# Optimization experiments

Measured on AMD Instinct MI355X. Metric: run time of the kernel, lower is better.

The kernel has to match this reference:

```python
import jax, jax.numpy as jnp
import numpy as np

B, T, D_IN, D_H, D_OUT = 32, 2048, 1024, 1024, 1024

def setup_inputs() -> dict:
    key = jax.random.key(0)
    k1, k2, k3, k4, k5 = jax.random.split(key, 5)
    s = jax.random.normal(k1, (B, D_IN), dtype=jnp.float32)
    h = jax.random.normal(k2, (B, T, D_H), dtype=jnp.float32)
    # params (original uses np.random.random, i.e. uniform [0,1); scale kept modest)
    W_a = jax.random.uniform(k3, (D_IN, D_OUT), dtype=jnp.float32)
    U_a = jax.random.uniform(k4, (D_H, D_OUT), dtype=jnp.float32)
    v_a = jax.random.uniform(k5, (D_OUT,), dtype=jnp.float32)
    return {"s": s, "h": h, "W_a": W_a, "U_a": U_a, "v_a": v_a}

def reference(s, h, W_a, U_a, v_a):
    # Bahdanau additive attention:
    # e_bt = v_a . tanh(s W_a + h_t U_a);  a = softmax_t(e);  c_b = sum_t a_bt h_bt
    u_a_h = jnp.einsum('bth,ho->bto', h, U_a)            # [B,T,O]
    w_a_s = jnp.einsum('bi,io->bo', s, W_a)[:, None, :]  # [B,1,O]
    e = jnp.einsum('bto,o->bt', jnp.tanh(w_a_s + u_a_h), v_a)  # [B,T]
    a = jax.nn.softmax(e, axis=-1)                       # [B,T]
    c = jnp.einsum('bt,bth->bh', a, h)                   # [B,H]
    return c
```

## Files before the change

### kernel.cpp

```cpp
#include <hip/hip_runtime.h>
#include <hip/hip_bf16.h>
#include <stdint.h>

#define Bb 32
#define Tt 2048
#define Dd 1024

typedef float    f32x4 __attribute__((ext_vector_type(4)));
typedef _Float16 f16x8 __attribute__((ext_vector_type(8)));
typedef uint32_t u32;

#define WS_A     131072
#define WS_EP    393216
#define WS_UT    4587520

__device__ __forceinline__ void gll16(const void* g, const void* lds) {
  __builtin_amdgcn_global_load_lds(
      (const __attribute__((address_space(1))) u32*)(uintptr_t)g,
      (__attribute__((address_space(3))) u32*)(uint32_t)(uintptr_t)lds,
      16, 0, 0);
}

__global__ __launch_bounds__(256) void k_ws(const float* __restrict__ s,
                                            const float* __restrict__ W,
                                            float* __restrict__ w2_ws) {
  const int b = blockIdx.x >> 2;
  const int o = (blockIdx.x & 3) * 256 + threadIdx.x;
  __shared__ float s_sh[Dd];
#pragma unroll
  for (int j = 0; j < 4; ++j)
    s_sh[threadIdx.x + 256 * j] = s[b * Dd + threadIdx.x + 256 * j];
  __syncthreads();
  float acc = 0.f;
#pragma unroll 8
  for (int i = 0; i < Dd; ++i) acc += s_sh[i] * W[(size_t)i * Dd + o];
  w2_ws[b * Dd + o] = 2.f * acc;
}

__global__ __launch_bounds__(256) void k_ut(const float* __restrict__ U,
                                            uint8_t* __restrict__ U_ts) {
  const int i0 = (blockIdx.x >> 4) * 64;
  const int o0 = (blockIdx.x & 15) * 64;
  __shared__ float tile[64][65];
  const int tx = threadIdx.x & 63;
  const int ty = threadIdx.x >> 6;
#pragma unroll
  for (int jj = 0; jj < 16; ++jj)
    tile[tx][ty + 4 * jj] = U[(size_t)(i0 + ty + 4 * jj) * Dd + o0 + tx];
  __syncthreads();
#pragma unroll
  for (int it = 0; it < 2; ++it) {
    const int g  = it * 256 + threadIdx.x;
    const int ol = g & 63;
    const int kg = g >> 6;
    const int o  = o0 + ol;
    const int k  = i0 + kg * 8;
    f16x8 r;
#pragma unroll
    for (int m = 0; m < 8; ++m) r[m] = (_Float16)tile[ol][kg * 8 + m];
    const int ob  = o >> 7, ks = k >> 6;
    const int o_l = o & 127, k_l = k & 63;
    const size_t byte = ((size_t)(ob * 16 + ks) << 14)
                      + (size_t)((k_l >> 5) * 8192 + (o_l >> 6) * 4096
                      + ((o_l >> 4) & 3) * 1024
                      + (((k_l >> 3) & 3) * 16 + (o_l & 15)) * 16);
    *(f16x8*)(U_ts + byte) = r;
  }
}

__global__ __launch_bounds__(256, 3) void k_e(const float* __restrict__ h,
                                              const uint8_t* __restrict__ U_ts,
                                              const float* __restrict__ w2_ws,
                                              const float* __restrict__ v_a,
                                              float* __restrict__ e_part) {
  const int blk = blockIdx.x;
  const int b   = blk >> 7;
  const int ob  = (blk >> 4) & 7;
  const int tb  = blk & 15;
  const int tid  = threadIdx.x;
  const int lane = tid & 63;
  const int w    = tid >> 6;
  const int hw   = w & 1;
  const int tw   = w >> 1;

  __shared__ __align__(16) uint8_t Al[16384];
  __shared__ __align__(16) uint8_t Bl[16384];
  __shared__ float w_sh[128], v_sh[128], exch[128];

  if (tid < 128) {
    w_sh[tid] = w2_ws[b * Dd + ob * 128 + tid];
    v_sh[tid] = v_a[ob * 128 + tid];
  }

  const float* hrow = h + ((size_t)(b * Tt + tb * 128 + (tid >> 3))) * Dd + (tid & 7) * 8;
  int baddr[4];
  {
    const int kk  = (tid & 7) >> 2;
    const int klo = (tid & 7) & 3;
#pragma unroll
    for (int j = 0; j < 4; ++j) {
      const int t_l = (tid >> 3) + 32 * j;
      baddr[j] = kk * 8192 + (t_l >> 6) * 4096 + ((t_l >> 4) & 3) * 1024
               + (klo * 16 + (t_l & 15)) * 16;
    }
  }
  const uint8_t* Ub = U_ts + ((size_t)(ob * 16) << 14);

  f32x4 acc[4][4] = {};

  for (int ks = 0; ks < 16; ++ks) {
    __syncthreads();
    f32x4 br[8];
#pragma unroll
    for (int j = 0; j < 4; ++j) {
      const float* p = hrow + (size_t)j * 32 * Dd + ks * 64;
      br[2 * j]     = *(const f32x4*)p;
      br[2 * j + 1] = *(const f32x4*)(p + 4);
    }
    {
      const uint8_t* As = Ub + ((size_t)ks << 14) + (size_t)tid * 16;
#pragma unroll
      for (int r = 0; r < 4; ++r)
        gll16(As + r * 4096, &Al[w * 1024 + r * 4096]);
    }
#pragma unroll
    for (int j = 0; j < 4; ++j) {
      f16x8 pk;
#pragma unroll
      for (int m = 0; m < 4; ++m) {
        pk[m]     = (_Float16)br[2 * j][m];
        pk[4 + m] = (_Float16)br[2 * j + 1][m];
      }
      *(f16x8*)(Bl + baddr[j]) = pk;
    }
    __syncthreads();
#pragma unroll
    for (int kk = 0; kk < 2; ++kk) {
      f16x8 af[4], bf[4];
#pragma unroll
      for (int n = 0; n < 4; ++n)
        af[n] = *(const f16x8*)(Al + kk * 8192 + hw * 4096 + n * 1024 + lane * 16);
#pragma unroll
      for (int m = 0; m < 4; ++m)
        bf[m] = *(const f16x8*)(Bl + kk * 8192 + tw * 4096 + m * 1024 + lane * 16);
#pragma unroll
      for (int m = 0; m < 4; ++m)
#pragma unroll
        for (int n = 0; n < 4; ++n)
          acc[m][n] = __builtin_amdgcn_mfma_f32_16x16x32_f16(af[n], bf[m], acc[m][n], 0, 0, 0);
    }
  }

  float ep[4] = {0.f, 0.f, 0.f, 0.f};
#pragma unroll
  for (int m = 0; m < 4; ++m)
#pragma unroll
    for (int n = 0; n < 4; ++n)
#pragma unroll
      for (int r = 0; r < 4; ++r) {
        const int o_loc = hw * 64 + n * 16 + ((lane >> 4) << 2) + r;
        const float x = __builtin_fmaf(acc[m][n][r], 2.f, w_sh[o_loc]);
        ep[m] += v_sh[o_loc] * (1.f - 2.f / (__expf(x) + 1.f));
      }
#pragma unroll
  for (int m = 0; m < 4; ++m) {
    ep[m] += __shfl_xor(ep[m], 16, 64);
    ep[m] += __shfl_xor(ep[m], 32, 64);
  }
  __syncthreads();
  if (hw == 1 && lane < 16) {
#pragma unroll
    for (int m = 0; m < 4; ++m) exch[tw * 64 + m * 16 + lane] = ep[m];
  }
  __syncthreads();
  if (hw == 0 && lane < 16) {
#pragma unroll
    for (int m = 0; m < 4; ++m) {
      const int t_loc = tw * 64 + m * 16 + lane;
      e_part[((size_t)(ob * Bb + b)) * Tt + tb * 128 + t_loc] = ep[m] + exch[t_loc];
    }
  }
}

__global__ __launch_bounds__(256) void k_sm(const float* __restrict__ e_part,
                                            float* __restrict__ a_ws) {
  const int b = blockIdx.x;
  const int lane = threadIdx.x & 63;
  const int wv = threadIdx.x >> 6;
  __shared__ float red[8];
  float ev[8];
  float m = -1e30f;
#pragma unroll
  for (int j = 0; j < 8; ++j) {
    const int t = threadIdx.x + 256 * j;
    float sv = 0.f;
#pragma unroll
    for (int o = 0; o < 8; ++o) sv += e_part[((size_t)(o * Bb + b)) * Tt + t];
    ev[j] = sv;
    m = fmaxf(m, sv);
  }
#pragma unroll
  for (int sft = 1; sft < 64; sft <<= 1) m = fmaxf(m, __shfl_xor(m, sft, 64));
  if (lane == 0) red[wv] = m;
  __syncthreads();
  m = fmaxf(fmaxf(red[0], red[1]), fmaxf(red[2], red[3]));
  float sum = 0.f;
#pragma unroll
  for (int j = 0; j < 8; ++j) { ev[j] = __expf(ev[j] - m); sum += ev[j]; }
#pragma unroll
  for (int sft = 1; sft < 64; sft <<= 1) sum += __shfl_xor(sum, sft, 64);
  if (lane == 0) red[4 + wv] = sum;
  __syncthreads();
  const float inv = 1.f / (red[4] + red[5] + red[6] + red[7]);
#pragma unroll
  for (int j = 0; j < 8; ++j) a_ws[b * Tt + threadIdx.x + 256 * j] = ev[j] * inv;
}

__global__ __launch_bounds__(256) void k_c1(const float* __restrict__ h,
                                            const float* __restrict__ a_ws,
                                            float* __restrict__ cpart) {
  const int b  = blockIdx.x >> 5;
  const int tc = blockIdx.x & 31;
  const int t0 = tc << 6;
  __shared__ float a_sh[64];
  if (threadIdx.x < 64) a_sh[threadIdx.x] = a_ws[b * Tt + t0 + threadIdx.x];
  __syncthreads();
  f32x4 acc = {0.f, 0.f, 0.f, 0.f};
  const float* hb = h + ((size_t)b * Tt + t0) * Dd + threadIdx.x * 4;
#pragma unroll 4
  for (int t = 0; t < 64; ++t) {
    const f32x4 hv = *(const f32x4*)(hb + (size_t)t * Dd);
    acc += a_sh[t] * hv;
  }
  *(f32x4*)(cpart + ((size_t)(tc * 32 + b) << 10) + threadIdx.x * 4) = acc;
}

__global__ __launch_bounds__(256) void k_c2(const float* __restrict__ cpart,
                                            float* __restrict__ out) {
  const int gid = blockIdx.x * 256 + threadIdx.x;
  const int b = gid >> 10;
  const int d = gid & 1023;
  float sv = 0.f;
#pragma unroll
  for (int tc = 0; tc < 32; ++tc) sv += cpart[((size_t)(tc * 32 + b) << 10) + d];
  out[gid] = sv;
}

extern "C" void kernel_launch(void* const* d_in, const int* in_sizes, int n_in,
                              void* d_out, int out_size, void* d_ws, size_t ws_size,
                              hipStream_t stream) {
  (void)in_sizes; (void)n_in; (void)out_size; (void)ws_size;
  const float* s  = (const float*)d_in[0];
  const float* h  = (const float*)d_in[1];
  const float* W  = (const float*)d_in[2];
  const float* U  = (const float*)d_in[3];
  const float* v  = (const float*)d_in[4];
  uint8_t* ws = (uint8_t*)d_ws;
  float*   w2_ws  = (float*)ws;
  float*   a_ws   = (float*)(ws + WS_A);
  float*   e_part = (float*)(ws + WS_EP);
  float*   cpart  = (float*)(ws + WS_EP);
  uint8_t* U_ts   = ws + WS_UT;

  k_ws<<<128, 256, 0, stream>>>(s, W, w2_ws);
  k_ut<<<256, 256, 0, stream>>>(U, U_ts);
  k_e <<<4096, 256, 0, stream>>>(h, U_ts, w2_ws, v, e_part);
  k_sm<<<Bb, 256, 0, stream>>>(e_part, a_ws);
  k_c1<<<1024, 256, 0, stream>>>(h, a_ws, cpart);
  k_c2<<<128, 256, 0, stream>>>(cpart, (float*)d_out);
}
```

Baseline: 343.6 us.

## Double-buffer U tiles in LDS, prefetch h into registers, swizzle B LDS

```diff
diff --git a/kernel.cpp b/kernel.cpp
--- a/kernel.cpp
+++ b/kernel.cpp
@@ -83,7 +83,7 @@
   const int hw   = w & 1;
   const int tw   = w >> 1;
 
-  __shared__ __align__(16) uint8_t Al[16384];
+  __shared__ __align__(16) uint8_t Al[2][16384];
   __shared__ __align__(16) uint8_t Bl[16384];
   __shared__ float w_sh[128], v_sh[128], exch[128];
 
@@ -97,59 +97,97 @@
   {
     const int kk  = (tid & 7) >> 2;
     const int klo = (tid & 7) & 3;
+    const int cw  = tid & 7;
 #pragma unroll
     for (int j = 0; j < 4; ++j) {
       const int t_l = (tid >> 3) + 32 * j;
       baddr[j] = kk * 8192 + (t_l >> 6) * 4096 + ((t_l >> 4) & 3) * 1024
-               + (klo * 16 + (t_l & 15)) * 16;
+               + (klo * 16 + ((t_l & 15) ^ cw)) * 16;
     }
   }
+  const int klo_r = lane >> 4;
+  const int rs0 = (klo_r * 16 + ((lane & 15) ^ klo_r)) * 16;
+  const int rs1 = (klo_r * 16 + ((lane & 15) ^ klo_r ^ 4)) * 16;
   const uint8_t* Ub = U_ts + ((size_t)(ob * 16) << 14);
 
   f32x4 acc[4][4] = {};
-
-  for (int ks = 0; ks < 16; ++ks) {
-    __syncthreads();
-    f32x4 br[8];
-#pragma unroll
-    for (int j = 0; j < 4; ++j) {
-      const float* p = hrow + (size_t)j * 32 * Dd + ks * 64;
-      br[2 * j]     = *(const f32x4*)p;
-      br[2 * j + 1] = *(const f32x4*)(p + 4);
-    }
-    {
-      const uint8_t* As = Ub + ((size_t)ks << 14) + (size_t)tid * 16;
-#pragma unroll
-      for (int r = 0; r < 4; ++r)
-        gll16(As + r * 4096, &Al[w * 1024 + r * 4096]);
-    }
-#pragma unroll
-    for (int j = 0; j < 4; ++j) {
-      f16x8 pk;
-#pragma unroll
-      for (int m = 0; m < 4; ++m) {
-        pk[m]     = (_Float16)br[2 * j][m];
-        pk[4 + m] = (_Float16)br[2 * j + 1][m];
-      }
-      *(f16x8*)(Bl + baddr[j]) = pk;
-    }
-    __syncthreads();
-#pragma unroll
-    for (int kk = 0; kk < 2; ++kk) {
-      f16x8 af[4], bf[4];
-#pragma unroll
-      for (int n = 0; n < 4; ++n)
-        af[n] = *(const f16x8*)(Al + kk * 8192 + hw * 4096 + n * 1024 + lane * 16);
-#pragma unroll
-      for (int m = 0; m < 4; ++m)
-        bf[m] = *(const f16x8*)(Bl + kk * 8192 + tw * 4096 + m * 1024 + lane * 16);
-#pragma unroll
-      for (int m = 0; m < 4; ++m)
-#pragma unroll
-        for (int n = 0; n < 4; ++n)
-          acc[m][n] = __builtin_amdgcn_mfma_f32_16x16x32_f16(af[n], bf[m], acc[m][n], 0, 0, 0);
-    }
-  }
+  f32x4 brA[8], brB[8];
+
+  {
+    const uint8_t* As = Ub + (size_t)tid * 16;
+    gll16(As,         &Al[0][w * 1024]);
+    gll16(As + 4096,  &Al[0][w * 1024 + 4096]);
+    gll16(As + 8192,  &Al[0][w * 1024 + 8192]);
+    gll16(As + 12288, &Al[0][w * 1024 + 12288]);
+  }
+#pragma unroll
+  for (int j = 0; j < 4; ++j) {
+    const float* p = hrow + (size_t)j * 32 * Dd;
+    brA[2 * j]     = *(const f32x4*)p;
+    brA[2 * j + 1] = *(const f32x4*)(p + 4);
+  }
+
+#define STEP(KS, CUR, brC, brN)                                               \
+  {                                                                           \
+    __builtin_amdgcn_sched_barrier(0);                                        \
+    __builtin_amdgcn_s_barrier();            \
+    __builtin_amdgcn_sched_barrier(0);                                        \
+    if ((KS) + 1 < 16) {                       \
+      const uint8_t* As = Ub + ((size_t)((KS) + 1) << 14) + (size_t)tid * 16; \
+      gll16(As,         &Al[(CUR) ^ 1][w * 1024]);                            \
+      gll16(As + 4096,  &Al[(CUR) ^ 1][w * 1024 + 4096]);                     \
+      gll16(As + 8192,  &Al[(CUR) ^ 1][w * 1024 + 8192]);                     \
+      gll16(As + 12288, &Al[(CUR) ^ 1][w * 1024 + 12288]);                    \
+    }                                                                         \
+    _Pragma("unroll")                        \
+    for (int j = 0; j < 4; ++j) {                                             \
+      f16x8 pk;                                                               \
+      _Pragma("unroll")                                                       \
+      for (int m2 = 0; m2 < 4; ++m2) {                                        \
+        pk[m2]     = (_Float16)brC[2 * j][m2];                                \
+        pk[4 + m2] = (_Float16)brC[2 * j + 1][m2];                            \
+      }                                                                       \
+      *(f16x8*)(Bl + baddr[j]) = pk;                                          \
+    }                                                                         \
+    if ((KS) + 1 < 16) {                         \
+      _Pragma("unroll")                                                       \
+      for (int j = 0; j < 4; ++j) {                                           \
+        const float* p = hrow + (size_t)j * 32 * Dd + ((KS) + 1) * 64;        \
+        brN[2 * j]     = *(const f32x4*)p;                                    \
+        brN[2 * j + 1] = *(const f32x4*)(p + 4);                              \
+      }                                                                       \
+    }                                                                         \
+    asm volatile("s_waitcnt lgkmcnt(0)" ::: "memory");    \
+    __builtin_amdgcn_sched_barrier(0);                                        \
+    __builtin_amdgcn_s_barrier();                                     \
+    __builtin_amdgcn_sched_barrier(0);                                        \
+    _Pragma("unroll")                                                         \
+    for (int kk = 0; kk < 2; ++kk) {                                          \
+      f16x8 af[4], bf[4];                                                     \
+      _Pragma("unroll")                                                       \
+      for (int n = 0; n < 4; ++n)                                             \
+        af[n] = *(const f16x8*)(&Al[CUR][0] + kk * 8192 + hw * 4096           \
+                                + n * 1024 + lane * 16);                      \
+      _Pragma("unroll")                                                       \
+      for (int m = 0; m < 4; ++m)                                             \
+        bf[m] = *(const f16x8*)(Bl + kk * 8192 + tw * 4096 + m * 1024         \
+                                + (kk ? rs1 : rs0));                          \
+      _Pragma("unroll")                                                       \
+      for (int m = 0; m < 4; ++m)                                             \
+        _Pragma("unroll")                                                     \
+        for (int n = 0; n < 4; ++n)                                           \
+          acc[m][n] = __builtin_amdgcn_mfma_f32_16x16x32_f16(af[n], bf[m],    \
+                                                             acc[m][n], 0, 0, 0); \
+    }                                                                         \
+  }
+
+#pragma unroll 1
+  for (int ks2 = 0; ks2 < 8; ++ks2) {
+    const int ks = ks2 * 2;
+    STEP(ks,     0, brA, brB)
+    STEP(ks + 1, 1, brB, brA)
+  }
+#undef STEP
 
   float ep[4] = {0.f, 0.f, 0.f, 0.f};
 #pragma unroll
```

Measured after the change: 524.0 us. +52.5%, slower.

## Widen k_e output tile to 256 and double-buffer U tiles with prefetch

Applied to the files above, without the earlier changes.

```diff
diff --git a/kernel.cpp b/kernel.cpp
--- a/kernel.cpp
+++ b/kernel.cpp
@@ -68,14 +68,14 @@
   }
 }
 
-__global__ __launch_bounds__(256, 3) void k_e(const float* __restrict__ h,
+__global__ __launch_bounds__(256, 2) void k_e(const float* __restrict__ h,
                                               const uint8_t* __restrict__ U_ts,
                                               const float* __restrict__ w2_ws,
                                               const float* __restrict__ v_a,
                                               float* __restrict__ e_part) {
   const int blk = blockIdx.x;
-  const int b   = blk >> 7;
-  const int ob  = (blk >> 4) & 7;
+  const int b   = blk >> 6;
+  const int obb = (blk >> 4) & 3;
   const int tb  = blk & 15;
   const int tid  = threadIdx.x;
   const int lane = tid & 63;
@@ -83,71 +83,89 @@
   const int hw   = w & 1;
   const int tw   = w >> 1;
 
-  __shared__ __align__(16) uint8_t Al[16384];
-  __shared__ __align__(16) uint8_t Bl[16384];
-  __shared__ float w_sh[128], v_sh[128], exch[128];
-
-  if (tid < 128) {
-    w_sh[tid] = w2_ws[b * Dd + ob * 128 + tid];
-    v_sh[tid] = v_a[ob * 128 + tid];
-  }
-
-  const float* hrow = h + ((size_t)(b * Tt + tb * 128 + (tid >> 3))) * Dd + (tid & 7) * 8;
-  int baddr[4];
+  __shared__ __align__(16) uint8_t Al[2][32768];
+  __shared__ float w_sh[256], v_sh[256], exch[128];
+
+  w_sh[tid] = w2_ws[b * Dd + obb * 256 + tid];
+  v_sh[tid] = v_a[obb * 256 + tid];
+  asm volatile("s_waitcnt vmcnt(0)" ::: "memory");
+
+  const int tile_i  = w >> 1;
+  const int segbase = (w & 1) * 8;
+  const uint8_t* Usrc = U_ts + ((size_t)((2 * obb + tile_i) * 16) << 14)
+                      + (size_t)segbase * 1024 + (size_t)lane * 16;
+  uint8_t* Adst0 = &Al[0][tile_i * 16384 + segbase * 1024];
+  uint8_t* Adst1 = &Al[1][tile_i * 16384 + segbase * 1024];
+
+  const float* hb = h + ((size_t)(b * Tt + tb * 128 + tw * 64 + (lane & 15))) * Dd
+                  + (lane >> 4) * 8;
+
+  f32x4 acc[4][8] = {};
+  f32x4 br[16];
+  f16x8 bf[8];
+
   {
-    const int kk  = (tid & 7) >> 2;
-    const int klo = (tid & 7) & 3;
-#pragma unroll
-    for (int j = 0; j < 4; ++j) {
-      const int t_l = (tid >> 3) + 32 * j;
-      baddr[j] = kk * 8192 + (t_l >> 6) * 4096 + ((t_l >> 4) & 3) * 1024
-               + (klo * 16 + (t_l & 15)) * 16;
-    }
-  }
-  const uint8_t* Ub = U_ts + ((size_t)(ob * 16) << 14);
-
-  f32x4 acc[4][4] = {};
-
+#pragma unroll
+    for (int q = 0; q < 8; ++q) gll16(Usrc + q * 1024, Adst0 + q * 1024);
+  }
+#pragma unroll
+  for (int kk = 0; kk < 2; ++kk)
+#pragma unroll
+    for (int m = 0; m < 4; ++m) {
+      const float* p = hb + (size_t)m * 16 * Dd + kk * 32;
+      br[kk * 8 + m * 2]     = *(const f32x4*)p;
+      br[kk * 8 + m * 2 + 1] = *(const f32x4*)(p + 4);
+    }
+  asm volatile("s_waitcnt lgkmcnt(0)" ::: "memory");
+
+#pragma unroll 1
   for (int ks = 0; ks < 16; ++ks) {
-    __syncthreads();
-    f32x4 br[8];
-#pragma unroll
-    for (int j = 0; j < 4; ++j) {
-      const float* p = hrow + (size_t)j * 32 * Dd + ks * 64;
-      br[2 * j]     = *(const f32x4*)p;
-      br[2 * j + 1] = *(const f32x4*)(p + 4);
-    }
-    {
-      const uint8_t* As = Ub + ((size_t)ks << 14) + (size_t)tid * 16;
-#pragma unroll
-      for (int r = 0; r < 4; ++r)
-        gll16(As + r * 4096, &Al[w * 1024 + r * 4096]);
-    }
-#pragma unroll
-    for (int j = 0; j < 4; ++j) {
-      f16x8 pk;
-#pragma unroll
-      for (int m = 0; m < 4; ++m) {
-        pk[m]     = (_Float16)br[2 * j][m];
-        pk[4 + m] = (_Float16)br[2 * j + 1][m];
+    const int p = ks & 1;
+    asm volatile("s_waitcnt vmcnt(16)" ::: "memory");
+    __builtin_amdgcn_sched_barrier(0);
+    __builtin_amdgcn_s_barrier();
+    __builtin_amdgcn_sched_barrier(0);
+    if (ks < 15) {
+      const uint8_t* src = Usrc + ((size_t)(ks + 1) << 14);
+      uint8_t* dst = p ? Adst0 : Adst1;
+#pragma unroll
+      for (int q = 0; q < 8; ++q) gll16(src + q * 1024, dst + q * 1024);
+    }
+#pragma unroll
+    for (int j = 0; j < 8; ++j) {
+      f16x8 t;
+#pragma unroll
+      for (int m2 = 0; m2 < 4; ++m2) {
+        t[m2]     = (_Float16)br[2 * j][m2];
+        t[4 + m2] = (_Float16)br[2 * j + 1][m2];
       }
-      *(f16x8*)(Bl + baddr[j]) = pk;
-    }
-    __syncthreads();
+      bf[j] = t;
+    }
+    __builtin_amdgcn_sched_barrier(0);
+    if (ks < 15) {
+#pragma unroll
+      for (int kk = 0; kk < 2; ++kk)
+#pragma unroll
+        for (int m = 0; m < 4; ++m) {
+          const float* pp = hb + (size_t)m * 16 * Dd + (ks + 1) * 64 + kk * 32;
+          br[kk * 8 + m * 2]     = *(const f32x4*)pp;
+          br[kk * 8 + m * 2 + 1] = *(const f32x4*)(pp + 4);
+        }
+    }
+    __builtin_amdgcn_sched_barrier(0);
+    const uint8_t* Ab = &Al[p][hw * 16384] + lane * 16;
 #pragma unroll
     for (int kk = 0; kk < 2; ++kk) {
-      f16x8 af[4], bf[4];
-#pragma unroll
-      for (int n = 0; n < 4; ++n)
-        af[n] = *(const f16x8*)(Al + kk * 8192 + hw * 4096 + n * 1024 + lane * 16);
+      f16x8 af[8];
+#pragma unroll
+      for (int n = 0; n < 8; ++n)
+        af[n] = *(const f16x8*)(Ab + kk * 8192 + (n >> 2) * 4096 + (n & 3) * 1024);
 #pragma unroll
       for (int m = 0; m < 4; ++m)
-        bf[m] = *(const f16x8*)(Bl + kk * 8192 + tw * 4096 + m * 1024 + lane * 16);
-#pragma unroll
-      for (int m = 0; m < 4; ++m)
-#pragma unroll
-        for (int n = 0; n < 4; ++n)
-          acc[m][n] = __builtin_amdgcn_mfma_f32_16x16x32_f16(af[n], bf[m], acc[m][n], 0, 0, 0);
+#pragma unroll
+        for (int n = 0; n < 8; ++n)
+          acc[m][n] = __builtin_amdgcn_mfma_f32_16x16x32_f16(af[n], bf[kk * 4 + m],
+                                                             acc[m][n], 0, 0, 0);
     }
   }
 
@@ -155,10 +173,10 @@
 #pragma unroll
   for (int m = 0; m < 4; ++m)
 #pragma unroll
-    for (int n = 0; n < 4; ++n)
+    for (int n = 0; n < 8; ++n)
 #pragma unroll
       for (int r = 0; r < 4; ++r) {
-        const int o_loc = hw * 64 + n * 16 + ((lane >> 4) << 2) + r;
+        const int o_loc = hw * 128 + n * 16 + ((lane >> 4) << 2) + r;
         const float x = __builtin_fmaf(acc[m][n][r], 2.f, w_sh[o_loc]);
         ep[m] += v_sh[o_loc] * (1.f - 2.f / (__expf(x) + 1.f));
       }
@@ -177,7 +195,7 @@
 #pragma unroll
     for (int m = 0; m < 4; ++m) {
       const int t_loc = tw * 64 + m * 16 + lane;
-      e_part[((size_t)(ob * Bb + b)) * Tt + tb * 128 + t_loc] = ep[m] + exch[t_loc];
+      e_part[((size_t)(obb * Bb + b)) * Tt + tb * 128 + t_loc] = ep[m] + exch[t_loc];
     }
   }
 }
@@ -195,7 +213,7 @@
     const int t = threadIdx.x + 256 * j;
     float sv = 0.f;
 #pragma unroll
-    for (int o = 0; o < 8; ++o) sv += e_part[((size_t)(o * Bb + b)) * Tt + t];
+    for (int o = 0; o < 4; ++o) sv += e_part[((size_t)(o * Bb + b)) * Tt + t];
     ev[j] = sv;
     m = fmaxf(m, sv);
   }
@@ -264,7 +282,7 @@
 
   k_ws<<<128, 256, 0, stream>>>(s, W, w2_ws);
   k_ut<<<256, 256, 0, stream>>>(U, U_ts);
-  k_e <<<4096, 256, 0, stream>>>(h, U_ts, w2_ws, v, e_part);
+  k_e <<<2048, 256, 0, stream>>>(h, U_ts, w2_ws, v, e_part);
   k_sm<<<Bb, 256, 0, stream>>>(e_part, a_ws);
   k_c1<<<1024, 256, 0, stream>>>(h, a_ws, cpart);
   k_c2<<<128, 256, 0, stream>>>(cpart, (float*)d_out);
```

New measurement: 549.1 us. 1.6x slower.

## Widen k_e tile to 256 outputs, prefetch h one step ahead, swizzle B LDS

Applied to the files above, without the earlier changes.

```diff
diff --git a/kernel.cpp b/kernel.cpp
--- a/kernel.cpp
+++ b/kernel.cpp
@@ -68,117 +68,145 @@
   }
 }
 
-__global__ __launch_bounds__(256, 3) void k_e(const float* __restrict__ h,
+__global__ __launch_bounds__(512, 3) void k_e(const float* __restrict__ h,
                                               const uint8_t* __restrict__ U_ts,
                                               const float* __restrict__ w2_ws,
                                               const float* __restrict__ v_a,
                                               float* __restrict__ e_part) {
   const int blk = blockIdx.x;
-  const int b   = blk >> 7;
-  const int ob  = (blk >> 4) & 7;
+  const int b   = blk >> 6;
+  const int obb = (blk >> 4) & 3;
   const int tb  = blk & 15;
   const int tid  = threadIdx.x;
   const int lane = tid & 63;
   const int w    = tid >> 6;
-  const int hw   = w & 1;
-  const int tw   = w >> 1;
-
-  __shared__ __align__(16) uint8_t Al[16384];
+  const int tw   = w >> 2;
+  const int ow   = w & 3;
+
+  __shared__ __align__(16) uint8_t Al[32768];
   __shared__ __align__(16) uint8_t Bl[16384];
-  __shared__ float w_sh[128], v_sh[128], exch[128];
-
-  if (tid < 128) {
-    w_sh[tid] = w2_ws[b * Dd + ob * 128 + tid];
-    v_sh[tid] = v_a[ob * 128 + tid];
-  }
-
-  const float* hrow = h + ((size_t)(b * Tt + tb * 128 + (tid >> 3))) * Dd + (tid & 7) * 8;
-  int baddr[4];
-  {
-    const int kk  = (tid & 7) >> 2;
-    const int klo = (tid & 7) & 3;
-#pragma unroll
-    for (int j = 0; j < 4; ++j) {
-      const int t_l = (tid >> 3) + 32 * j;
-      baddr[j] = kk * 8192 + (t_l >> 6) * 4096 + ((t_l >> 4) & 3) * 1024
-               + (klo * 16 + (t_l & 15)) * 16;
-    }
-  }
-  const uint8_t* Ub = U_ts + ((size_t)(ob * 16) << 14);
+  __shared__ float exch[512];
+
+  const uint8_t* Asrc[4];
+#pragma unroll
+  for (int q = 0; q < 4; ++q)
+    Asrc[q] = U_ts + ((size_t)((obb * 2 + (q >> 1)) * 16) << 14)
+            + (size_t)(((q & 1) * 512 + w * 64 + lane) * 16);
+
+  const float* hb[2];
+  int baddr[2];
+#pragma unroll
+  for (int j = 0; j < 2; ++j) {
+    const int u   = j * 512 + tid;
+    const int t_l = u >> 3;
+    const int kg  = u & 7;
+    hb[j] = h + ((size_t)(b * Tt + tb * 128 + t_l)) * Dd + kg * 8;
+    const int kk  = kg >> 2;
+    const int klo = kg & 3;
+    baddr[j] = kk * 8192 + (t_l >> 6) * 4096 + ((t_l >> 4) & 3) * 1024
+             + (klo * 16 + ((t_l & 15) ^ kg)) * 16;
+  }
+
+  const int aoff = (ow >> 1) * 16384 + (ow & 1) * 4096 + lane * 16;
+  const int klo_r = lane >> 4;
+  const int rs0 = (klo_r * 16 + ((lane & 15) ^ klo_r)) * 16;
+  const int rs1 = (klo_r * 16 + ((lane & 15) ^ klo_r ^ 4)) * 16;
+  const int boff = tw * 4096;
 
   f32x4 acc[4][4] = {};
-
+  f32x4 br[4];
+  f16x8 pk[2];
+
+#pragma unroll
+  for (int j = 0; j < 2; ++j) {
+    br[2 * j]     = *(const f32x4*)(hb[j]);
+    br[2 * j + 1] = *(const f32x4*)(hb[j] + 4);
+  }
+#pragma unroll
+  for (int j = 0; j < 2; ++j) {
+    f16x8 t;
+#pragma unroll
+    for (int m2 = 0; m2 < 4; ++m2) {
+      t[m2]     = (_Float16)br[2 * j][m2];
+      t[4 + m2] = (_Float16)br[2 * j + 1][m2];
+    }
+    pk[j] = t;
+  }
+
+#pragma unroll 1
   for (int ks = 0; ks < 16; ++ks) {
     __syncthreads();
-    f32x4 br[8];
-#pragma unroll
-    for (int j = 0; j < 4; ++j) {
-      const float* p = hrow + (size_t)j * 32 * Dd + ks * 64;
-      br[2 * j]     = *(const f32x4*)p;
-      br[2 * j + 1] = *(const f32x4*)(p + 4);
-    }
-    {
-      const uint8_t* As = Ub + ((size_t)ks << 14) + (size_t)tid * 16;
-#pragma unroll
-      for (int r = 0; r < 4; ++r)
-        gll16(As + r * 4096, &Al[w * 1024 + r * 4096]);
-    }
-#pragma unroll
-    for (int j = 0; j < 4; ++j) {
-      f16x8 pk;
-#pragma unroll
-      for (int m = 0; m < 4; ++m) {
-        pk[m]     = (_Float16)br[2 * j][m];
-        pk[4 + m] = (_Float16)br[2 * j + 1][m];
-      }
-      *(f16x8*)(Bl + baddr[j]) = pk;
-    }
+#pragma unroll
+    for (int q = 0; q < 4; ++q)
+      gll16(Asrc[q] + ((size_t)ks << 14), Al + q * 8192 + w * 1024);
+#pragma unroll
+    for (int j = 0; j < 2; ++j) *(f16x8*)(Bl + baddr[j]) = pk[j];
     __syncthreads();
+    const int kso = (ks < 15 ? ks + 1 : 0) * 64;
+#pragma unroll
+    for (int j = 0; j < 2; ++j) {
+      br[2 * j]     = *(const f32x4*)(hb[j] + kso);
+      br[2 * j + 1] = *(const f32x4*)(hb[j] + kso + 4);
+    }
 #pragma unroll
     for (int kk = 0; kk < 2; ++kk) {
       f16x8 af[4], bf[4];
 #pragma unroll
       for (int n = 0; n < 4; ++n)
-        af[n] = *(const f16x8*)(Al + kk * 8192 + hw * 4096 + n * 1024 + lane * 16);
+        af[n] = *(const f16x8*)(Al + aoff + kk * 8192 + n * 1024);
 #pragma unroll
       for (int m = 0; m < 4; ++m)
-        bf[m] = *(const f16x8*)(Bl + kk * 8192 + tw * 4096 + m * 1024 + lane * 16);
+        bf[m] = *(const f16x8*)(Bl + boff + kk * 8192 + m * 1024 + (kk ? rs1 : rs0));
 #pragma unroll
       for (int m = 0; m < 4; ++m)
 #pragma unroll
         for (int n = 0; n < 4; ++n)
-          acc[m][n] = __builtin_amdgcn_mfma_f32_16x16x32_f16(af[n], bf[m], acc[m][n], 0, 0, 0);
-    }
-  }
-
+          acc[m][n] = __builtin_amdgcn_mfma_f32_16x16x32_f16(af[n], bf[m],
+                                                             acc[m][n], 0, 0, 0);
+    }
+#pragma unroll
+    for (int j = 0; j < 2; ++j) {
+      f16x8 t;
+#pragma unroll
+      for (int m2 = 0; m2 < 4; ++m2) {
+        t[m2]     = (_Float16)br[2 * j][m2];
+        t[4 + m2] = (_Float16)br[2 * j + 1][m2];
+      }
+      pk[j] = t;
+    }
+  }
+
+  const float* wbase = w2_ws + b * Dd + obb * 256;
+  const float* vbase = v_a + obb * 256;
   float ep[4] = {0.f, 0.f, 0.f, 0.f};
 #pragma unroll
-  for (int m = 0; m < 4; ++m)
-#pragma unroll
-    for (int n = 0; n < 4; ++n)
+  for (int n = 0; n < 4; ++n) {
+    const int og = ow * 64 + n * 16 + ((lane >> 4) << 2);
+    const f32x4 w4 = *(const f32x4*)(wbase + og);
+    const f32x4 v4 = *(const f32x4*)(vbase + og);
+#pragma unroll
+    for (int m = 0; m < 4; ++m)
 #pragma unroll
       for (int r = 0; r < 4; ++r) {
-        const int o_loc = hw * 64 + n * 16 + ((lane >> 4) << 2) + r;
-        const float x = __builtin_fmaf(acc[m][n][r], 2.f, w_sh[o_loc]);
-        ep[m] += v_sh[o_loc] * (1.f - 2.f / (__expf(x) + 1.f));
+        const float x = __builtin_fmaf(acc[m][n][r], 2.f, w4[r]);
+        ep[m] += v4[r] * (1.f - 2.f / (__expf(x) + 1.f));
       }
+  }
 #pragma unroll
   for (int m = 0; m < 4; ++m) {
     ep[m] += __shfl_xor(ep[m], 16, 64);
     ep[m] += __shfl_xor(ep[m], 32, 64);
   }
   __syncthreads();
-  if (hw == 1 && lane < 16) {
-#pragma unroll
-    for (int m = 0; m < 4; ++m) exch[tw * 64 + m * 16 + lane] = ep[m];
-  }
-  __syncthreads();
-  if (hw == 0 && lane < 16) {
-#pragma unroll
-    for (int m = 0; m < 4; ++m) {
-      const int t_loc = tw * 64 + m * 16 + lane;
-      e_part[((size_t)(ob * Bb + b)) * Tt + tb * 128 + t_loc] = ep[m] + exch[t_loc];
-    }
+  if (lane < 16) {
+#pragma unroll
+    for (int m = 0; m < 4; ++m)
+      exch[ow * 128 + tw * 64 + m * 16 + lane] = ep[m];
+  }
+  __syncthreads();
+  if (tid < 128) {
+    const float sv = exch[tid] + exch[128 + tid] + exch[256 + tid] + exch[384 + tid];
+    e_part[((size_t)(obb * Bb + b)) * Tt + tb * 128 + tid] = sv;
   }
 }
 
@@ -195,7 +223,7 @@
     const int t = threadIdx.x + 256 * j;
     float sv = 0.f;
 #pragma unroll
-    for (int o = 0; o < 8; ++o) sv += e_part[((size_t)(o * Bb + b)) * Tt + t];
+    for (int o = 0; o < 4; ++o) sv += e_part[((size_t)(o * Bb + b)) * Tt + t];
     ev[j] = sv;
     m = fmaxf(m, sv);
   }
@@ -264,7 +292,7 @@
 
   k_ws<<<128, 256, 0, stream>>>(s, W, w2_ws);
   k_ut<<<256, 256, 0, stream>>>(U, U_ts);
-  k_e <<<4096, 256, 0, stream>>>(h, U_ts, w2_ws, v, e_part);
+  k_e <<<2048, 512, 0, stream>>>(h, U_ts, w2_ws, v, e_part);
   k_sm<<<Bb, 256, 0, stream>>>(e_part, a_ws);
   k_c1<<<1024, 256, 0, stream>>>(h, a_ws, cpart);
   k_c2<<<128, 256, 0, stream>>>(cpart, (float*)d_out);
```

New measurement: 283.0 us. 1.21x faster.
